# Kernel optimization log

Measured on AMD Instinct MI355X. Metric: run time of the kernel, lower is better.

Reference implementation:

```python
import jax, jax.numpy as jnp
import numpy as np

_SAMPLING_EPS = 1e-5


def setup_inputs() -> dict:
    key = jax.random.key(0)
    k0, k1, k2, k3, k4, k5, k6 = jax.random.split(key, 7)
    T, D, V, B = 8192, 4096, 32000, 64  # total tokens, hidden, vocab, num seqs
    hidden_states = jax.random.normal(k0, (T, D), jnp.float32)
    embedding = jax.random.normal(k1, (V, D), jnp.float32) * 0.02
    last_token_indices = jnp.sort(jax.random.randint(k2, (B,), 0, T)).astype(jnp.int64)
    temperatures = jax.random.uniform(k3, (B,), jnp.float32)  # in (0,1)
    top_ps = jax.random.uniform(k4, (B,), jnp.float32)
    top_ks = jax.random.randint(k5, (B,), 1, 1000).astype(jnp.int64)
    u = jax.random.uniform(k6, (B,), jnp.float32)  # inverse-CDF sample draw
    return {
        "hidden_states": hidden_states,
        "embedding": embedding,
        "temperatures": temperatures,
        "top_ps": top_ps,
        "u": u,
        "last_token_indices": last_token_indices,
        "top_ks": top_ks,
    }


def reference(hidden_states, embedding, temperatures, top_ps, u,
              last_token_indices, top_ks):
    V = embedding.shape[0]
    # _prune_hidden_states: keep last token of each sequence -> [B, D]
    h = hidden_states[last_token_indices]
    # _get_logits: [B, V]
    logits = jnp.einsum("bd,vd->bv", h, embedding)
    # temperature scaling (temps < eps treated as 1.0, greedy handled upstream)
    temps = jnp.where(temperatures < _SAMPLING_EPS, 1.0, temperatures)
    logits = logits / temps[:, None]
    probs = jax.nn.softmax(logits.astype(jnp.float32), axis=-1)

    # sort descending once; do top-k and top-p filtering in sorted space
    order = jnp.argsort(-probs, axis=-1)                 # [B, V]
    sorted_p = jnp.take_along_axis(probs, order, axis=-1)
    k = jnp.clip(top_ks, 1, V).astype(jnp.int32)
    kth = jnp.take_along_axis(sorted_p, (k - 1)[:, None], axis=-1)  # [B,1]
    f = jnp.where(sorted_p >= kth, sorted_p, 0.0)        # top-k filter
    cum = jnp.cumsum(f, axis=-1)
    # keep index i iff cumsum up to i-1 <= top_p (first element always kept)
    keep_p = ((cum - f) <= top_ps[:, None]) | (top_ps[:, None] >= 1.0 - _SAMPLING_EPS)
    f = jnp.where(keep_p, f, 0.0)
    total = jnp.sum(f, axis=-1, keepdims=True)
    # fallback to unfiltered probs if everything got zeroed
    f = jnp.where(total > 0, f, sorted_p)
    total = jnp.sum(f, axis=-1, keepdims=True)

    # multinomial via inverse CDF in sorted space
    cdf = jnp.cumsum(f, axis=-1)
    j = jnp.sum(cdf < u[:, None] * total, axis=-1)
    j = jnp.clip(j, 0, V - 1)
    tokens = jnp.take_along_axis(order, j[:, None], axis=-1).reshape(-1)

    # filtered normalized probs back in token order (for inspection/grads)
    inv = jnp.argsort(order, axis=-1)
    probs_final = jnp.take_along_axis(f / total, inv, axis=-1)
    return tokens, probs_final
```

## Files before the change

kernel.cpp:

```cpp
#include <hip/hip_runtime.h>
#include <stdint.h>

#define D_DIM 4096
#define V_DIM 32000
#define B_SEQ 64
#define MAXC 2048
#define SPLITK 4
#define KCH 1024

typedef __attribute__((ext_vector_type(8))) short short8;
typedef __attribute__((ext_vector_type(4))) float f32x4;

#define H1_OFF     0u
#define H2_OFF     131072u
#define H3_OFF     262144u
#define LOGITS_OFF 393216u
#define PART_OFF   2441216u

#define GLD16(gsrc, ldst) \
    __builtin_amdgcn_global_load_lds((const __attribute__((address_space(1))) unsigned*)(gsrc), \
                                     (__attribute__((address_space(3))) unsigned*)(ldst), 16, 0, 0)

__device__ __forceinline__ unsigned f2key(float x) {
    unsigned u = __float_as_uint(x);
    return (u & 0x80000000u) ? ~u : (u | 0x80000000u);
}
__device__ __forceinline__ float key2f(unsigned k) {
    unsigned u = (k & 0x80000000u) ? (k & 0x7FFFFFFFu) : ~k;
    return __uint_as_float(u);
}
__device__ __forceinline__ void split3(float x, ushort& a, ushort& b, ushort& c) {
    unsigned u = __float_as_uint(x);
    a = (ushort)(u >> 16);
    float r1 = x - __uint_as_float(u & 0xFFFF0000u);
    unsigned u2 = __float_as_uint(r1);
    b = (ushort)(u2 >> 16);
    float r2 = r1 - __uint_as_float(u2 & 0xFFFF0000u);
    c = (ushort)(__float_as_uint(r2) >> 16);
}

__global__ void k_prep(const float* __restrict__ hs, const int* __restrict__ lti,
                       ushort* __restrict__ h1, ushort* __restrict__ h2,
                       ushort* __restrict__ h3) {
    int b = blockIdx.x >> 2;
    int quarter = blockIdx.x & 3;
    int base = quarter * (D_DIM / 16);
    const float4* src = (const float4*)(hs + (size_t)lti[b] * D_DIM);
    ushort4* d1 = (ushort4*)(h1 + (size_t)b * D_DIM);
    ushort4* d2 = (ushort4*)(h2 + (size_t)b * D_DIM);
    ushort4* d3 = (ushort4*)(h3 + (size_t)b * D_DIM);
    int i = base + threadIdx.x;
    float4 v = src[i];
    float x[4] = {v.x, v.y, v.z, v.w};
    ushort l1[4], l2[4], l3[4];
#pragma unroll
    for (int j = 0; j < 4; ++j) split3(x[j], l1[j], l2[j], l3[j]);
    d1[i] = make_ushort4(l1[0], l1[1], l1[2], l1[3]);
    d2[i] = make_ushort4(l2[0], l2[1], l2[2], l2[3]);
    d3[i] = make_ushort4(l3[0], l3[1], l3[2], l3[3]);
}

__device__ __forceinline__ void splitB(const float4& x0, const float4& x1,
                                       short8& b1, short8& b2, short8& b3) {
    float xf[8] = {x0.x, x0.y, x0.z, x0.w, x1.x, x1.y, x1.z, x1.w};
#pragma unroll
    for (int j = 0; j < 8; ++j) {
        ushort u1, u2, u3;
        split3(xf[j], u1, u2, u3);
        b1[j] = (short)u1; b2[j] = (short)u2; b3[j] = (short)u3;
    }
}

__global__ __launch_bounds__(256, 2) void k_gemm(const ushort* __restrict__ h1,
                                                 const ushort* __restrict__ h2,
                                                 const ushort* __restrict__ h3,
                                                 const float* __restrict__ emb,
                                                 float* __restrict__ part) {
    __shared__ __align__(16) float  sB[8192];
    __shared__ __align__(16) ushort sA1[4096];
    __shared__ __align__(16) ushort sA2[4096];
    __shared__ __align__(16) ushort sA3[4096];
    const int tid = threadIdx.x;
    const int w = tid >> 6, lane = tid & 63, lrow = lane & 15, q = lane >> 4;
    const int kc = blockIdx.y;
    const int vbase = blockIdx.x * 128;
    const size_t kbase = (size_t)kc * KCH;

    f32x4 acc[4][2];
#pragma unroll
    for (int mf = 0; mf < 4; ++mf)
#pragma unroll
        for (int nf = 0; nf < 2; ++nf)
#pragma unroll
            for (int r = 0; r < 4; ++r) acc[mf][nf][r] = 0.f;

    const float* srcB[8];
#pragma unroll
    for (int j = 0; j < 8; ++j) {
        int row = w * 4 + j * 16 + (lane >> 4);
        unsigned c16 = (((unsigned)(lane & 15)) << 4) ^ (((unsigned)(row & 7)) << 4);
        srcB[j] = emb + (size_t)(vbase + row) * D_DIM + kbase + (c16 >> 2);
    }
    const ushort* srcA1[2]; const ushort* srcA2[2]; const ushort* srcA3[2];
#pragma unroll
    for (int j = 0; j < 2; ++j) {
        int row = w * 8 + j * 32 + (lane >> 3);
        unsigned c16 = (((unsigned)(lane & 7)) << 4) ^ (((unsigned)(row & 7)) << 4);
        size_t off = (size_t)row * D_DIM + kbase + (c16 >> 1);
        srcA1[j] = h1 + off; srcA2[j] = h2 + off; srcA3[j] = h3 + off;
    }
    const unsigned ldst = (unsigned)(w * 1024);

    for (int k0 = 0; k0 < KCH; k0 += 64) {
        if (k0) __syncthreads();
#pragma unroll
        for (int j = 0; j < 8; ++j)
            GLD16(srcB[j] + k0, (char*)sB + ldst + j * 4096);
#pragma unroll
        for (int j = 0; j < 2; ++j) {
            GLD16(srcA1[j] + k0, (char*)sA1 + ldst + j * 4096);
            GLD16(srcA2[j] + k0, (char*)sA2 + ldst + j * 4096);
            GLD16(srcA3[j] + k0, (char*)sA3 + ldst + j * 4096);
        }
        __syncthreads();
#pragma unroll
        for (int s = 0; s < 2; ++s) {
            short8 vb1[2], vb2[2], vb3[2];
#pragma unroll
            for (int nf = 0; nf < 2; ++nf) {
                unsigned brow = (unsigned)(w * 32 + nf * 16 + lrow);
                const char* bb = (const char*)sB + brow * 256u;
                unsigned bswz = (brow & 7u) << 4;
                unsigned binner = (unsigned)(s * 128 + q * 32);
                float4 bf0 = *(const float4*)(bb + (binner ^ bswz));
                float4 bf1 = *(const float4*)(bb + ((binner + 16u) ^ bswz));
                splitB(bf0, bf1, vb1[nf], vb2[nf], vb3[nf]);
            }
#pragma unroll
            for (int mf = 0; mf < 4; ++mf) {
                unsigned arow = (unsigned)(mf * 16 + lrow);
                unsigned abyte = arow * 128u
                               + (((unsigned)(s * 64 + q * 16)) ^ ((arow & 7u) << 4));
                short8 a1 = *(const short8*)((const char*)sA1 + abyte);
                short8 a2 = *(const short8*)((const char*)sA2 + abyte);
                short8 a3 = *(const short8*)((const char*)sA3 + abyte);
#pragma unroll
                for (int nf = 0; nf < 2; ++nf) {
                    acc[mf][nf] = __builtin_amdgcn_mfma_f32_16x16x32_bf16(a1, vb1[nf], acc[mf][nf], 0, 0, 0);
                    acc[mf][nf] = __builtin_amdgcn_mfma_f32_16x16x32_bf16(a1, vb2[nf], acc[mf][nf], 0, 0, 0);
                    acc[mf][nf] = __builtin_amdgcn_mfma_f32_16x16x32_bf16(a2, vb1[nf], acc[mf][nf], 0, 0, 0);
                    acc[mf][nf] = __builtin_amdgcn_mfma_f32_16x16x32_bf16(a2, vb2[nf], acc[mf][nf], 0, 0, 0);
                    acc[mf][nf] = __builtin_amdgcn_mfma_f32_16x16x32_bf16(a1, vb3[nf], acc[mf][nf], 0, 0, 0);
                    acc[mf][nf] = __builtin_amdgcn_mfma_f32_16x16x32_bf16(a3, vb1[nf], acc[mf][nf], 0, 0, 0);
                }
            }
        }
    }
    float* pout = part + (size_t)kc * (B_SEQ * V_DIM);
#pragma unroll
    for (int mf = 0; mf < 4; ++mf)
#pragma unroll
        for (int r = 0; r < 4; ++r) {
            int m = mf * 16 + q * 4 + r;
#pragma unroll
            for (int nf = 0; nf < 2; ++nf)
                pout[(size_t)m * V_DIM + vbase + w * 32 + nf * 16 + lrow] = acc[mf][nf][r];
        }
}

__device__ __forceinline__ float4 f4add(float4 a, float4 b) {
    return make_float4(a.x + b.x, a.y + b.y, a.z + b.z, a.w + b.w);
}

__global__ void k_reduce(const float* __restrict__ part,
                         const float* __restrict__ temps,
                         float* __restrict__ logits,
                         float* __restrict__ out_probs) {
    const int b = blockIdx.y;
    float t = temps[b];
    if (t < 1e-5f) t = 1.0f;
    const float inv = 1.0f / t;
    const float4* p0 = (const float4*)(part + 0 * (size_t)(B_SEQ * V_DIM) + (size_t)b * V_DIM);
    const float4* p1 = (const float4*)(part + 1 * (size_t)(B_SEQ * V_DIM) + (size_t)b * V_DIM);
    const float4* p2 = (const float4*)(part + 2 * (size_t)(B_SEQ * V_DIM) + (size_t)b * V_DIM);
    const float4* p3 = (const float4*)(part + 3 * (size_t)(B_SEQ * V_DIM) + (size_t)b * V_DIM);
    float4* lo = (float4*)(logits + (size_t)b * V_DIM);
    float4* po = (float4*)(out_probs + (size_t)b * V_DIM);
    const float4 z4 = make_float4(0.f, 0.f, 0.f, 0.f);
    for (int i = blockIdx.x * 256 + threadIdx.x; i < V_DIM / 4; i += 2048) {
        float4 s = f4add(f4add(f4add(p0[i], p1[i]), p2[i]), p3[i]);
        lo[i] = make_float4(s.x * inv, s.y * inv, s.z * inv, s.w * inv);
        po[i] = z4;
    }
}

__global__ __launch_bounds__(512) void k_sample(const float* __restrict__ logits,
                                                const int* __restrict__ tks,
                                                const float* __restrict__ tps,
                                                const float* __restrict__ uu,
                                                float* __restrict__ out_tok,
                                                float* __restrict__ out_probs) {
    const int b = blockIdx.x, t = threadIdx.x;
    const float* lr = logits + (size_t)b * V_DIM;
    __shared__ unsigned hist[2048];
    __shared__ unsigned redu[512];
    __shared__ float redf[512];
    __shared__ unsigned long long cand[MAXC];
    __shared__ float sp[MAXC];
    __shared__ unsigned s_sel1, s_ab1, s_thr, s_nc, s_ab2, s_kthkey;
    __shared__ float s_m, s_Z, s_tot;
    __shared__ int s_cnt, s_L, s_tok, s_nk;

    int k = tks[b];
    if (k < 1) k = 1;
    if (k > V_DIM) k = V_DIM;

    for (int i = t; i < 2048; i += 512) hist[i] = 0u;
    __syncthreads();
    unsigned km = 0u;
    for (int v = t; v < V_DIM; v += 512) {
        unsigned key = f2key(lr[v]);
        km = max(km, key);
        atomicAdd(&hist[key >> 21], 1u);
    }
    redu[t] = km;
    __syncthreads();
    for (int s = 256; s > 0; s >>= 1) {
        if (t < s) redu[t] = max(redu[t], redu[t + s]);
        __syncthreads();
    }
    if (t == 0) s_m = key2f(redu[0]);
    __syncthreads();
    float m = s_m;
    redu[t] = hist[4 * t] + hist[4 * t + 1] + hist[4 * t + 2] + hist[4 * t + 3];
    __syncthreads();
    if (t == 0) {
        unsigned acc = 0; int g = 0; bool found = false;
        for (int g0 = 511; g0 >= 0 && !found; g0 -= 8) {
            unsigned v[8];
#pragma unroll
            for (int j = 0; j < 8; ++j) v[j] = redu[g0 - j];
#pragma unroll
            for (int j = 0; j < 8; ++j) {
                if (acc + v[j] >= (unsigned)k) { g = g0 - j; found = true; break; }
                acc += v[j];
            }
        }
        int sel = 4 * g;
        for (int bk = 4 * g + 3; bk >= 4 * g; --bk) {
            unsigned h = hist[bk];
            if (acc + h >= (unsigned)k) { sel = bk; break; }
            acc += h;
        }
        s_sel1 = (unsigned)sel; s_ab1 = acc;
    }
    __syncthreads();
    unsigned sel1 = s_sel1, ab1 = s_ab1;

    for (int i = t; i < 2048; i += 512) hist[i] = 0u;
    __syncthreads();
    float es = 0.f;
    for (int v = t; v < V_DIM; v += 512) {
        float f = lr[v];
        es += expf(f - m);
        unsigned key = f2key(f);
        if ((key >> 21) == sel1) atomicAdd(&hist[(key >> 10) & 2047u], 1u);
    }
    redf[t] = es;
    __syncthreads();
    for (int s = 256; s > 0; s >>= 1) {
        if (t < s) redf[t] += redf[t + s];
        __syncthreads();
    }
    if (t == 0) s_Z = redf[0];
    __syncthreads();
    redu[t] = hist[4 * t] + hist[4 * t + 1] + hist[4 * t + 2] + hist[4 * t + 3];
    __syncthreads();
    if (t == 0) {
        unsigned kk = (unsigned)k - ab1;
        unsigned acc = 0; int g = 0; bool found = false;
        for (int g0 = 511; g0 >= 0 && !found; g0 -= 8) {
            unsigned v[8];
#pragma unroll
            for (int j = 0; j < 8; ++j) v[j] = redu[g0 - j];
#pragma unroll
            for (int j = 0; j < 8; ++j) {
                if (acc + v[j] >= kk) { g = g0 - j; found = true; break; }
                acc += v[j];
            }
        }
        int sel = 4 * g;
        for (int bk = 4 * g + 3; bk >= 4 * g; --bk) {
            unsigned h = hist[bk];
            if (acc + h >= kk) { sel = bk; break; }
            acc += h;
        }
        s_ab2 = ab1 + acc;
        s_thr = (sel1 << 21) | ((unsigned)sel << 10);
        s_nc = ab1 + acc + hist[sel];
    }
    __syncthreads();
    unsigned thr = s_thr;

    if (s_nc > (unsigned)MAXC) {
        for (int i = t; i < 1024; i += 512) hist[i] = 0u;
        __syncthreads();
        for (int v = t; v < V_DIM; v += 512) {
            unsigned key = f2key(lr[v]);
            if ((key & 0xFFFFFC00u) == thr) atomicAdd(&hist[key & 1023u], 1u);
        }
        __syncthreads();
        if (t == 0) {
            unsigned kk = (unsigned)k - s_ab2;
            unsigned acc = 0; int sel = 0;
            for (int bk = 1023; bk >= 0; --bk) {
                unsigned h = hist[bk];
                if (acc + h >= kk) { sel = bk; break; }
                acc += h;
            }
            s_thr = thr | (unsigned)sel;
        }
        __syncthreads();
        thr = s_thr;
    }

    if (t == 0) s_cnt = 0;
    for (int i = t; i < MAXC; i += 512) cand[i] = 0xFFFFFFFFFFFFFFFFULL;
    __syncthreads();
    for (int v = t; v < V_DIM; v += 512) {
        unsigned key = f2key(lr[v]);
        if (key >= thr) {
            int p = atomicAdd(&s_cnt, 1);
            if (p < MAXC) cand[p] = (((unsigned long long)(~key)) << 32) | (unsigned)v;
        }
    }
    __syncthreads();
    int n = s_cnt; if (n > MAXC) n = MAXC;
    const int np2 = (n <= 1) ? 1 : (1 << (32 - __clz(n - 1)));

    for (unsigned size = 2; size <= (unsigned)np2; size <<= 1)
        for (unsigned stride = size >> 1; stride > 0; stride >>= 1) {
            for (unsigned i = t; i < (unsigned)np2; i += 512) {
                unsigned j = i ^ stride;
                if (j > i) {
                    unsigned long long a = cand[i], c = cand[j];
                    bool up = ((i & size) == 0);
                    if (up ? (a > c) : (a < c)) { cand[i] = c; cand[j] = a; }
                }
            }
            __syncthreads();
        }
    float Z = s_Z;
    for (int i = t; i < n; i += 512) {
        unsigned key = ~(unsigned)(cand[i] >> 32);
        sp[i] = expf(key2f(key) - m) / Z;
    }
    for (int i = n + t; i < MAXC; i += 512) sp[i] = 0.f;
    if (t == 0) s_kthkey = ~(unsigned)(cand[k - 1] >> 32);
    __syncthreads();

    unsigned kthkey = s_kthkey;
    int cnt = 0;
    for (int i = t; i < n; i += 512)
        if ((~(unsigned)(cand[i] >> 32)) >= kthkey) cnt++;
    redu[t] = (unsigned)cnt;
    __syncthreads();
    for (int s = 256; s > 0; s >>= 1) {
        if (t < s) redu[t] += redu[t + s];
        __syncthreads();
    }
    if (t == 0) s_nk = (int)redu[0];
    __syncthreads();

    if (t == 0) {
        float top_p = tps[b];
        bool keepall = (top_p >= 1.0f - 1e-5f);
        int limit = min(n, s_nk);
        float c = 0.f; int L = limit; bool done = false;
        for (int i0 = 0; i0 < limit && !done; i0 += 8) {
            float v[8];
#pragma unroll
            for (int j = 0; j < 8; ++j) v[j] = sp[i0 + j];
#pragma unroll
            for (int j = 0; j < 8; ++j) {
                int i = i0 + j;
                if (i >= limit) { done = true; break; }
                float cum = c + v[j];
                if (!keepall && !((cum - v[j]) <= top_p)) { L = i; done = true; break; }
                c = cum;
            }
        }
        float total = c;
        float target = uu[b] * total;
        float c2 = 0.f; int jj = L - 1; done = false;
        for (int i0 = 0; i0 < L && !done; i0 += 8) {
            float v[8];
#pragma unroll
            for (int j = 0; j < 8; ++j) v[j] = sp[i0 + j];
#pragma unroll
            for (int j = 0; j < 8; ++j) {
                int i = i0 + j;
                if (i >= L) { done = true; break; }
                c2 += v[j];
                if (!(c2 < target)) { jj = i; done = true; break; }
            }
        }
        s_tok = (int)(cand[jj] & 0xFFFFFFFFULL);
        s_L = L; s_tot = total;
        out_tok[b] = (float)s_tok;
    }
    __syncthreads();
    int L = s_L; float total = s_tot;
    for (int i = t; i < L; i += 512) {
        unsigned v = (unsigned)(cand[i] & 0xFFFFFFFFULL);
        out_probs[(size_t)b * V_DIM + v] = sp[i] / total;
    }
}

extern "C" void kernel_launch(void* const* d_in, const int* in_sizes, int n_in,
                              void* d_out, int out_size, void* d_ws, size_t ws_size,
                              hipStream_t stream) {
    const float* hs    = (const float*)d_in[0];
    const float* emb   = (const float*)d_in[1];
    const float* temps = (const float*)d_in[2];
    const float* tps   = (const float*)d_in[3];
    const float* uu    = (const float*)d_in[4];
    const int*   lti   = (const int*)d_in[5];
    const int*   tks   = (const int*)d_in[6];

    float* ws = (float*)d_ws;
    ushort* h1 = (ushort*)(ws + H1_OFF);
    ushort* h2 = (ushort*)(ws + H2_OFF);
    ushort* h3 = (ushort*)(ws + H3_OFF);
    float* logits = ws + LOGITS_OFF;
    float* part   = ws + PART_OFF;

    float* out_tok   = (float*)d_out;
    float* out_probs = (float*)d_out + B_SEQ;

    k_prep<<<B_SEQ * 4, 256, 0, stream>>>(hs, lti, h1, h2, h3);
    k_gemm<<<dim3(V_DIM / 128, SPLITK), 256, 0, stream>>>(h1, h2, h3, emb, part);
    k_reduce<<<dim3(8, B_SEQ), 256, 0, stream>>>(part, temps, logits, out_probs);
    k_sample<<<B_SEQ, 512, 0, stream>>>(logits, tks, tps, uu, out_tok, out_probs);
}
```

Before: 299.4 us.

## Widen sampling kernel to 1024 threads with float4 logit scans

The per-sequence sampling kernel now runs 1024 threads instead of 512 and reads logits as float4 in the histogram and candidate passes. It also always runs the third radix-select pass, which removes the conditional branch and the full candidate-buffer initialisation, and pads only up to the next power of two before the bitonic sort. The aim is more memory parallelism and fewer instructions in the latency-bound 64-block sampling stage. The cost is an extra full pass over the logits when the candidate count was already small, plus more contention on the shared-memory histogram atomics.

Measured after the change: 331.9 us. 10.9% more time.

```diff
diff --git a/kernel.cpp b/kernel.cpp
--- a/kernel.cpp
+++ b/kernel.cpp
@@ -194,20 +194,21 @@
     }
 }
 
-__global__ __launch_bounds__(512) void k_sample(const float* __restrict__ logits,
-                                                const int* __restrict__ tks,
-                                                const float* __restrict__ tps,
-                                                const float* __restrict__ uu,
-                                                float* __restrict__ out_tok,
-                                                float* __restrict__ out_probs) {
+__global__ __launch_bounds__(1024) void k_sample(const float* __restrict__ logits,
+                                                 const int* __restrict__ tks,
+                                                 const float* __restrict__ tps,
+                                                 const float* __restrict__ uu,
+                                                 float* __restrict__ out_tok,
+                                                 float* __restrict__ out_probs) {
     const int b = blockIdx.x, t = threadIdx.x;
     const float* lr = logits + (size_t)b * V_DIM;
+    const float4* lr4 = (const float4*)lr;
     __shared__ unsigned hist[2048];
-    __shared__ unsigned redu[512];
+    __shared__ unsigned redu[1024];
     __shared__ float redf[512];
     __shared__ unsigned long long cand[MAXC];
     __shared__ float sp[MAXC];
-    __shared__ unsigned s_sel1, s_ab1, s_thr, s_nc, s_ab2, s_kthkey;
+    __shared__ unsigned s_sel1, s_ab1, s_thr, s_ab2, s_kthkey;
     __shared__ float s_m, s_Z, s_tot;
     __shared__ int s_cnt, s_L, s_tok, s_nk;
 
@@ -215,28 +216,33 @@
     if (k < 1) k = 1;
     if (k > V_DIM) k = V_DIM;
 
-    for (int i = t; i < 2048; i += 512) hist[i] = 0u;
+    for (int i = t; i < 2048; i += 1024) hist[i] = 0u;
     __syncthreads();
     unsigned km = 0u;
-    for (int v = t; v < V_DIM; v += 512) {
-        unsigned key = f2key(lr[v]);
-        km = max(km, key);
-        atomicAdd(&hist[key >> 21], 1u);
+    for (int i = t; i < V_DIM / 4; i += 1024) {
+        float4 f = lr4[i];
+        float xf[4] = {f.x, f.y, f.z, f.w};
+#pragma unroll
+        for (int j = 0; j < 4; ++j) {
+            unsigned key = f2key(xf[j]);
+            km = max(km, key);
+            atomicAdd(&hist[key >> 21], 1u);
+        }
     }
     redu[t] = km;
     __syncthreads();
-    for (int s = 256; s > 0; s >>= 1) {
+    for (int s = 512; s > 0; s >>= 1) {
         if (t < s) redu[t] = max(redu[t], redu[t + s]);
         __syncthreads();
     }
     if (t == 0) s_m = key2f(redu[0]);
     __syncthreads();
     float m = s_m;
-    redu[t] = hist[4 * t] + hist[4 * t + 1] + hist[4 * t + 2] + hist[4 * t + 3];
+    redu[t] = hist[2 * t] + hist[2 * t + 1];
     __syncthreads();
     if (t == 0) {
         unsigned acc = 0; int g = 0; bool found = false;
-        for (int g0 = 511; g0 >= 0 && !found; g0 -= 8) {
+        for (int g0 = 1023; g0 >= 0 && !found; g0 -= 8) {
             unsigned v[8];
 #pragma unroll
             for (int j = 0; j < 8; ++j) v[j] = redu[g0 - j];
@@ -246,8 +252,8 @@
                 acc += v[j];
             }
         }
-        int sel = 4 * g;
-        for (int bk = 4 * g + 3; bk >= 4 * g; --bk) {
+        int sel = 2 * g;
+        for (int bk = 2 * g + 1; bk >= 2 * g; --bk) {
             unsigned h = hist[bk];
             if (acc + h >= (unsigned)k) { sel = bk; break; }
             acc += h;
@@ -257,16 +263,22 @@
     __syncthreads();
     unsigned sel1 = s_sel1, ab1 = s_ab1;
 
-    for (int i = t; i < 2048; i += 512) hist[i] = 0u;
-    __syncthreads();
-    float es = 0.f;
-    for (int v = t; v < V_DIM; v += 512) {
-        float f = lr[v];
-        es += expf(f - m);
-        unsigned key = f2key(f);
-        if ((key >> 21) == sel1) atomicAdd(&hist[(key >> 10) & 2047u], 1u);
-    }
-    redf[t] = es;
+    for (int i = t; i < 2048; i += 1024) hist[i] = 0u;
+    __syncthreads();
+    for (int i = t; i < V_DIM / 4; i += 1024) {
+        float4 f = lr4[i];
+        float xf[4] = {f.x, f.y, f.z, f.w};
+#pragma unroll
+        for (int j = 0; j < 4; ++j) {
+            unsigned key = f2key(xf[j]);
+            if ((key >> 21) == sel1) atomicAdd(&hist[(key >> 10) & 2047u], 1u);
+        }
+    }
+    if (t < 512) {
+        float es = 0.f;
+        for (int v = t; v < V_DIM; v += 512) es += expf(lr[v] - m);
+        redf[t] = es;
+    }
     __syncthreads();
     for (int s = 256; s > 0; s >>= 1) {
         if (t < s) redf[t] += redf[t + s];
@@ -274,12 +286,12 @@
     }
     if (t == 0) s_Z = redf[0];
     __syncthreads();
-    redu[t] = hist[4 * t] + hist[4 * t + 1] + hist[4 * t + 2] + hist[4 * t + 3];
+    redu[t] = hist[2 * t] + hist[2 * t + 1];
     __syncthreads();
     if (t == 0) {
         unsigned kk = (unsigned)k - ab1;
         unsigned acc = 0; int g = 0; bool found = false;
-        for (int g0 = 511; g0 >= 0 && !found; g0 -= 8) {
+        for (int g0 = 1023; g0 >= 0 && !found; g0 -= 8) {
             unsigned v[8];
 #pragma unroll
             for (int j = 0; j < 8; ++j) v[j] = redu[g0 - j];
@@ -289,58 +301,65 @@
                 acc += v[j];
             }
         }
-        int sel = 4 * g;
-        for (int bk = 4 * g + 3; bk >= 4 * g; --bk) {
+        int sel = 2 * g;
+        for (int bk = 2 * g + 1; bk >= 2 * g; --bk) {
             unsigned h = hist[bk];
             if (acc + h >= kk) { sel = bk; break; }
             acc += h;
         }
         s_ab2 = ab1 + acc;
         s_thr = (sel1 << 21) | ((unsigned)sel << 10);
-        s_nc = ab1 + acc + hist[sel];
     }
     __syncthreads();
     unsigned thr = s_thr;
 
-    if (s_nc > (unsigned)MAXC) {
-        for (int i = t; i < 1024; i += 512) hist[i] = 0u;
-        __syncthreads();
-        for (int v = t; v < V_DIM; v += 512) {
-            unsigned key = f2key(lr[v]);
+    if (t < 1024) hist[t] = 0u;
+    __syncthreads();
+    for (int i = t; i < V_DIM / 4; i += 1024) {
+        float4 f = lr4[i];
+        float xf[4] = {f.x, f.y, f.z, f.w};
+#pragma unroll
+        for (int j = 0; j < 4; ++j) {
+            unsigned key = f2key(xf[j]);
             if ((key & 0xFFFFFC00u) == thr) atomicAdd(&hist[key & 1023u], 1u);
         }
-        __syncthreads();
-        if (t == 0) {
-            unsigned kk = (unsigned)k - s_ab2;
-            unsigned acc = 0; int sel = 0;
-            for (int bk = 1023; bk >= 0; --bk) {
-                unsigned h = hist[bk];
-                if (acc + h >= kk) { sel = bk; break; }
-                acc += h;
-            }
-            s_thr = thr | (unsigned)sel;
-        }
-        __syncthreads();
-        thr = s_thr;
-    }
-
-    if (t == 0) s_cnt = 0;
-    for (int i = t; i < MAXC; i += 512) cand[i] = 0xFFFFFFFFFFFFFFFFULL;
-    __syncthreads();
-    for (int v = t; v < V_DIM; v += 512) {
-        unsigned key = f2key(lr[v]);
-        if (key >= thr) {
-            int p = atomicAdd(&s_cnt, 1);
-            if (p < MAXC) cand[p] = (((unsigned long long)(~key)) << 32) | (unsigned)v;
+    }
+    __syncthreads();
+    if (t == 0) {
+        unsigned kk = (unsigned)k - s_ab2;
+        unsigned acc = 0; int sel = 0;
+        for (int bk = 1023; bk >= 0; --bk) {
+            unsigned h = hist[bk];
+            if (acc + h >= kk) { sel = bk; break; }
+            acc += h;
+        }
+        s_thr = thr | (unsigned)sel;
+        s_cnt = 0;
+    }
+    __syncthreads();
+    thr = s_thr;
+
+    for (int i = t; i < V_DIM / 4; i += 1024) {
+        float4 f = lr4[i];
+        float xf[4] = {f.x, f.y, f.z, f.w};
+#pragma unroll
+        for (int j = 0; j < 4; ++j) {
+            unsigned key = f2key(xf[j]);
+            if (key >= thr) {
+                int p = atomicAdd(&s_cnt, 1);
+                if (p < MAXC) cand[p] = (((unsigned long long)(~key)) << 32) | (unsigned)(4 * i + j);
+            }
         }
     }
     __syncthreads();
     int n = s_cnt; if (n > MAXC) n = MAXC;
     const int np2 = (n <= 1) ? 1 : (1 << (32 - __clz(n - 1)));
+    for (int i = n + t; i < np2; i += 1024) cand[i] = 0xFFFFFFFFFFFFFFFFULL;
+    __syncthreads();
 
     for (unsigned size = 2; size <= (unsigned)np2; size <<= 1)
         for (unsigned stride = size >> 1; stride > 0; stride >>= 1) {
-            for (unsigned i = t; i < (unsigned)np2; i += 512) {
+            for (unsigned i = t; i < (unsigned)np2; i += 1024) {
                 unsigned j = i ^ stride;
                 if (j > i) {
                     unsigned long long a = cand[i], c = cand[j];
@@ -351,21 +370,21 @@
             __syncthreads();
         }
     float Z = s_Z;
-    for (int i = t; i < n; i += 512) {
+    for (int i = t; i < n; i += 1024) {
         unsigned key = ~(unsigned)(cand[i] >> 32);
         sp[i] = expf(key2f(key) - m) / Z;
     }
-    for (int i = n + t; i < MAXC; i += 512) sp[i] = 0.f;
+    for (int i = n + t; i < MAXC; i += 1024) sp[i] = 0.f;
     if (t == 0) s_kthkey = ~(unsigned)(cand[k - 1] >> 32);
     __syncthreads();
 
     unsigned kthkey = s_kthkey;
     int cnt = 0;
-    for (int i = t; i < n; i += 512)
+    for (int i = t; i < n; i += 1024)
         if ((~(unsigned)(cand[i] >> 32)) >= kthkey) cnt++;
     redu[t] = (unsigned)cnt;
     __syncthreads();
-    for (int s = 256; s > 0; s >>= 1) {
+    for (int s = 512; s > 0; s >>= 1) {
         if (t < s) redu[t] += redu[t + s];
         __syncthreads();
     }
@@ -411,7 +430,7 @@
     }
     __syncthreads();
     int L = s_L; float total = s_tot;
-    for (int i = t; i < L; i += 512) {
+    for (int i = t; i < L; i += 1024) {
         unsigned v = (unsigned)(cand[i] & 0xFFFFFFFFULL);
         out_probs[(size_t)b * V_DIM + v] = sp[i] / total;
     }
@@ -441,5 +460,5 @@
     k_prep<<<B_SEQ * 4, 256, 0, stream>>>(hs, lti, h1, h2, h3);
     k_gemm<<<dim3(V_DIM / 128, SPLITK), 256, 0, stream>>>(h1, h2, h3, emb, part);
     k_reduce<<<dim3(8, B_SEQ), 256, 0, stream>>>(part, temps, logits, out_probs);
-    k_sample<<<B_SEQ, 512, 0, stream>>>(logits, tks, tps, uu, out_tok, out_probs);
-}
+    k_sample<<<B_SEQ, 1024, 0, stream>>>(logits, tks, tps, uu, out_tok, out_probs);
+}
```
